# Kernel optimization log

Hardware: AMD Instinct MI355X
Metric: run time of the kernel (lower is better)

Reference implementation:

```python
import jax, jax.numpy as jnp
import numpy as np

N_BINS = 64
INPUT_DIM = 8
R = 1.2
BOUND = 10.0
BETA = 1e-06
N = 2097152


def _mesh_and_elmt():
    m = N_BINS / 2
    idx = jnp.arange(N_BINS + 1, dtype=jnp.float32) - m
    x1L = BOUND * (R - 1.0) / (R ** m - 1.0)
    xr = (1.0 - R ** jnp.abs(idx)) / (1.0 - R)
    xr = jnp.where(idx >= 0, x1L * xr, -x1L * xr)
    xr = (xr + BOUND) / (2.0 * BOUND)
    mesh = jnp.concatenate([jnp.zeros((1,), jnp.float32), xr[1:-1], jnp.ones((1,), jnp.float32)])  # [n_bins+1]
    elmt = mesh[1:] - mesh[:-1]  # [n_bins]
    return mesh, elmt


def _pdf_normalize(p, elmt):
    # pdf: [n_bins+1, d]; F_ref: [n_bins, d] cumulative bin integrals
    p0 = jnp.full((1, INPUT_DIM), BETA, jnp.float32)
    ep = jnp.exp(p)
    px = ep * ((elmt[:-1] + elmt[1:]) / 2.0)[:, None]
    scale = (1.0 - (elmt[0] + elmt[-1]) * BETA / 2.0) / jnp.sum(px, 0, keepdims=True)
    px = scale * ep
    pdf = jnp.concatenate([p0, px, p0], 0)
    cell = (pdf[:-1] + pdf[1:]) / 2.0 * elmt[:, None]  # [n_bins, d]
    F_ref = jnp.concatenate([jnp.zeros((1, INPUT_DIM), jnp.float32),
                             jnp.cumsum(cell, 0)[:N_BINS - 1]], 0)
    return pdf, F_ref


def setup_inputs() -> dict:
    key = jax.random.key(0)
    k1, k2 = jax.random.split(key)
    x = jax.random.normal(k1, (N, INPUT_DIM), dtype=jnp.float32)
    logdet = jnp.zeros((N, 1), dtype=jnp.float32)
    p = jax.random.normal(k2, (N_BINS - 1, INPUT_DIM), dtype=jnp.float32)
    return {"x": x, "logdet": logdet, "p": p}


def reference(x, logdet, p):
    mesh, elmt = _mesh_and_elmt()
    pdf, F_ref = _pdf_normalize(p, elmt)

    xs = (x + BOUND) / (2.0 * BOUND)  # [N, d] in [0,1] for covered points
    k = jnp.searchsorted(mesh, xs, side='right') - 1  # [N, d]
    cover = (k >= 0) & (k <= N_BINS - 1)
    k = jnp.clip(k, 0, N_BINS - 1)
    col = jnp.arange(INPUT_DIM)[None, :]

    v1 = pdf[k, col]            # [N, d]
    v2 = pdf[k + 1, col]
    xm = xs - mesh[k]
    h = elmt[k]
    F_pre = F_ref[k, col]

    y = jnp.where(cover, F_pre + xm * xm / 2.0 * (v2 - v1) / h + xm * v1, xs)
    dld = jnp.where(cover, xm * (v2 - v1) / h + v1, 1.0)
    logdet = logdet + jnp.sum(jnp.log(dld), -1, keepdims=True)

    y = y * 2.0 * BOUND - BOUND
    y = jnp.where(y > BOUND, BETA * (y - BOUND) + BOUND, y)
    logdet = logdet + jnp.sum(jnp.log(jnp.where(y > BOUND, BETA, 1.0)), -1, keepdims=True)
    y = jnp.where(y < -BOUND, BETA * (y + BOUND) - BOUND, y)
    logdet = logdet + jnp.sum(jnp.log(jnp.where(y < -BOUND, BETA, 1.0)), -1, keepdims=True)
    return y, logdet
```

## Files before the change

kernel.cpp:

```cpp
#include <hip/hip_runtime.h>
#include <math.h>

#define NDIM   8
#define NBINS  64
#define LOG_BETA   (-13.815510557964274f)
#define LN2F       0.69314718055994531f
#define ALPHA      34.0821892f
#define INV_LOG2R  3.80178401692393f
#define L2R        0.26303440583379378f

typedef float f32x4 __attribute__((ext_vector_type(4)));

__global__ __launch_bounds__(256, 8) void cdfq_fused(const float* __restrict__ x,
                                                     const float* __restrict__ logdet_in,
                                                     const float* __restrict__ p,
                                                     float* __restrict__ y_out,
                                                     float* __restrict__ ld_out,
                                                     int n)
{
    __shared__ float4 stbl[NDIM * NBINS];

    const int t  = threadIdx.x;
    const int T  = gridDim.x * blockDim.x;
    const int i0 = blockIdx.x * blockDim.x + t;
    const int G  = 2 * n;
    const int iters = G / T;
    const f32x4* xv4 = (const f32x4*)x;

    f32x4 X0, X1, X2; float L0, L1, Lc2;
    if (iters > 0) { X0 = xv4[i0];         L0  = logdet_in[i0 >> 1]; }
    if (iters > 1) { X1 = xv4[i0 + T];     L1  = logdet_in[(i0 + T) >> 1]; }
    if (iters > 2) { X2 = xv4[i0 + 2 * T]; Lc2 = logdet_in[(i0 + 2 * T) >> 1]; }
    __builtin_amdgcn_sched_barrier(0);

    {
        const int lane = t & 63;
        const int w    = t >> 6;
        const float pw32 = exp2f(32.0f * L2R);
        const float inv  = 0.5f / (pw32 - 1.0f);
        auto meshf = [&](float tt) {
            float fidx = tt - 32.0f;
            float pw = exp2f(fabsf(fidx) * L2R);
            float r  = (pw - 1.0f) * inv;
            return 0.5f + ((fidx >= 0.0f) ? r : -r);
        };
        const float m0  = meshf((float)lane);
        const float m1  = meshf((float)(lane + 1));
        const float el  = m1 - m0;
        const float el1 = __shfl_down(el, 1);
        const float e0e63 = 2.0f * (meshf(1.0f) - meshf(0.0f));

#pragma unroll
        for (int dd = 0; dd < 2; ++dd) {
            const int d = 2 * w + dd;
            float ep = 0.0f;
            if (lane < 63) ep = __expf(p[lane * NDIM + d]);
            float s = ep * 0.5f * (el + el1);
#pragma unroll
            for (int off = 32; off; off >>= 1) s += __shfl_xor(s, off);
            const float scale = (1.0f - e0e63 * 5e-7f) / s;
            const float epu = __shfl_up(ep, 1);
            const float pdl = (lane == 0)  ? 1e-6f : scale * epu;
            const float pdn = (lane == 63) ? 1e-6f : scale * ep;
            const float cell = 0.5f * (pdl + pdn) * el;
            float v = cell;
#pragma unroll
            for (int off = 1; off < 64; off <<= 1) {
                float u = __shfl_up(v, off);
                if (lane >= off) v += u;
            }
            stbl[(d << 6) | lane] = make_float4(pdl, (pdn - pdl) / el, v - cell, m0);
        }
    }
    __syncthreads();

    const float4* tbl = &stbl[((i0 & 1) << 2) << 6];
    const bool evenlane = ((i0 & 1) == 0);

    auto body = [&](f32x4 Xv, float Lin, int g) {
        float yd[4];
        float contrib;

        float mx = fmaxf(fmaxf(fabsf(Xv[0]), fabsf(Xv[1])),
                         fmaxf(fabsf(Xv[2]), fabsf(Xv[3])));

        if (!__any(mx >= 10.0f)) {
            float dd4[4];
#pragma unroll
            for (int dl = 0; dl < 4; ++dl) {
                float xo = Xv[dl];
                float xs = fmaf(xo, 0.05f, 0.5f);
                float gg = __log2f(fmaf(ALPHA, fabsf(xo), 1.0f)) * INV_LOG2R;
                int jf = (int)fminf(gg, 31.0f);
                int k  = ((xo >= 0.0f) ? 32 : 31) ^ jf;

                f32x4 tv = *(const f32x4*)&tbl[(dl << 6) + k];
                float xm = xs - tv[3];
                yd[dl]  = fmaf(fmaf(xm, fmaf(0.5f * xm, tv[1], tv[0]), tv[2]),
                               20.0f, -10.0f);
                dd4[dl] = fmaf(xm, tv[1], tv[0]);
            }
            contrib = (__log2f(dd4[0] * dd4[1]) + __log2f(dd4[2] * dd4[3])) * LN2F;
        } else {
            float dd4[4];
            float extra = 0.0f;
#pragma unroll
            for (int dl = 0; dl < 4; ++dl) {
                float xo = Xv[dl];
                float xs = fmaf(xo, 0.05f, 0.5f);
                float gg = __log2f(fmaf(ALPHA, fabsf(xo), 1.0f)) * INV_LOG2R;
                int jf = (int)fminf(gg, 31.0f);
                int k  = ((xo >= 0.0f) ? 32 : 31) ^ jf;

                f32x4 tv = *(const f32x4*)&tbl[(dl << 6) + k];
                float xm = xs - tv[3];
                bool cov = (fabsf(xo) < 10.0f);

                float yc = fmaf(xm, fmaf(0.5f * xm, tv[1], tv[0]), tv[2]);
                float dv = fmaf(xm, tv[1], tv[0]);
                float yy = cov ? yc : xs;
                dd4[dl]  = cov ? dv : 1.0f;

                yy = fmaf(yy, 20.0f, -10.0f);
                if (yy > 10.0f)  { yy = fmaf(1e-6f, yy - 10.0f, 10.0f);  extra += LOG_BETA; }
                if (yy < -10.0f) { yy = fmaf(1e-6f, yy + 10.0f, -10.0f); extra += LOG_BETA; }
                yd[dl] = yy;
            }
            contrib = fmaf(__log2f(dd4[0] * dd4[1]) + __log2f(dd4[2] * dd4[3]),
                           LN2F, extra);
        }

        float cross = __shfl_xor(contrib, 1);

        f32x4 yv = { yd[0], yd[1], yd[2], yd[3] };
        __builtin_nontemporal_store(yv, (f32x4*)y_out + g);
        if (evenlane)
            __builtin_nontemporal_store(Lin + contrib + cross, ld_out + (g >> 1));
    };

    for (int j = 0; j < iters; ++j) {
        f32x4 Xn; float Ln;
        const bool more = (j + 3 < iters);
        if (more) {
            int gx = i0 + (j + 3) * T;
            Xn = xv4[gx];
            Ln = logdet_in[gx >> 1];
        }
        __builtin_amdgcn_sched_barrier(0);

        body(X0, L0, i0 + j * T);

        X0 = X1; L0 = L1;
        X1 = X2; L1 = Lc2;
        if (more) { X2 = Xn; Lc2 = Ln; }
    }

    for (int g = i0 + iters * T; g < G; g += T) {
        body(xv4[g], logdet_in[g >> 1], g);
    }
}

extern "C" void kernel_launch(void* const* d_in, const int* in_sizes, int n_in,
                              void* d_out, int out_size, void* d_ws, size_t ws_size,
                              hipStream_t stream) {
    const float* x      = (const float*)d_in[0];
    const float* logdet = (const float*)d_in[1];
    const float* p      = (const float*)d_in[2];

    const int n = in_sizes[1];
    float* y_out  = (float*)d_out;
    float* ld_out = (float*)d_out + (size_t)n * NDIM;

    const int block = 256;
    int grid = 2048;
    if ((long long)grid * block > 2LL * n) grid = (2 * n + block - 1) / block;
    cdfq_fused<<<grid, block, 0, stream>>>(x, logdet, p, y_out, ld_out, n);
}
```

Measured before the change: 137.3 us.

## Prefetch all eight per-thread tiles upfront in a shape-specialized fast path

Adds a fast path for the case where each thread handles exactly eight vec4 elements. In that case all eight x vectors and logdet values are loaded before the table build, replacing the three-deep rotating prefetch, and the compute loop is fully unrolled. The point is to have every global load in flight while the shared-memory table is built, hiding memory latency. This needs more registers, so launch bounds drop from 8 to 7 blocks per CU; other shapes fall back to a plain grid-stride loop with no prefetch.

```diff
diff --git a/kernel.cpp b/kernel.cpp
--- a/kernel.cpp
+++ b/kernel.cpp
@@ -11,7 +11,7 @@
 
 typedef float f32x4 __attribute__((ext_vector_type(4)));
 
-__global__ __launch_bounds__(256, 8) void cdfq_fused(const float* __restrict__ x,
+__global__ __launch_bounds__(256, 7) void cdfq_fused(const float* __restrict__ x,
                                                      const float* __restrict__ logdet_in,
                                                      const float* __restrict__ p,
                                                      float* __restrict__ y_out,
@@ -25,12 +25,18 @@
     const int i0 = blockIdx.x * blockDim.x + t;
     const int G  = 2 * n;
     const int iters = G / T;
+    const bool fast = (iters == 8) && (iters * T == G);
     const f32x4* xv4 = (const f32x4*)x;
 
-    f32x4 X0, X1, X2; float L0, L1, Lc2;
-    if (iters > 0) { X0 = xv4[i0];         L0  = logdet_in[i0 >> 1]; }
-    if (iters > 1) { X1 = xv4[i0 + T];     L1  = logdet_in[(i0 + T) >> 1]; }
-    if (iters > 2) { X2 = xv4[i0 + 2 * T]; Lc2 = logdet_in[(i0 + 2 * T) >> 1]; }
+    f32x4 X[8]; float L[8];
+    if (fast) {
+#pragma unroll
+        for (int j = 0; j < 8; ++j) {
+            int g = i0 + j * T;
+            X[j] = xv4[g];
+            L[j] = logdet_in[g >> 1];
+        }
+    }
     __builtin_amdgcn_sched_barrier(0);
 
     {
@@ -138,25 +144,13 @@
             __builtin_nontemporal_store(Lin + contrib + cross, ld_out + (g >> 1));
     };
 
-    for (int j = 0; j < iters; ++j) {
-        f32x4 Xn; float Ln;
-        const bool more = (j + 3 < iters);
-        if (more) {
-            int gx = i0 + (j + 3) * T;
-            Xn = xv4[gx];
-            Ln = logdet_in[gx >> 1];
-        }
-        __builtin_amdgcn_sched_barrier(0);
-
-        body(X0, L0, i0 + j * T);
-
-        X0 = X1; L0 = L1;
-        X1 = X2; L1 = Lc2;
-        if (more) { X2 = Xn; Lc2 = Ln; }
-    }
-
-    for (int g = i0 + iters * T; g < G; g += T) {
-        body(xv4[g], logdet_in[g >> 1], g);
+    if (fast) {
+#pragma unroll
+        for (int j = 0; j < 8; ++j)
+            body(X[j], L[j], i0 + j * T);
+    } else {
+        for (int g = i0; g < G; g += T)
+            body(xv4[g], logdet_in[g >> 1], g);
     }
 }
 
```

After: 156.4 us. 1.14x slower.
